# Performance work log

Hardware: AMD Instinct MI355X
Metric: run time of the kernel (lower is better)

## Reference

```python
import jax, jax.numpy as jnp
import numpy as np

N0, N1, N2, N3 = 262144, 65536, 16384, 4096
EPS = 1e-5  # BatchNorm1d default eps


def setup_inputs() -> dict:
    key = jax.random.key(0)
    ks = jax.random.split(key, 10)
    f0 = jax.random.normal(ks[0], (N0, 64), dtype=jnp.float32)
    f1 = jax.random.normal(ks[1], (N1, 128), dtype=jnp.float32)
    f2 = jax.random.normal(ks[2], (N2, 256), dtype=jnp.float32)
    f3 = jax.random.normal(ks[3], (N3, 512), dtype=jnp.float32)
    # upsampling indices: finer level gathers from coarser level
    idx0 = jax.random.randint(ks[4], (N2,), 0, N3, dtype=jnp.int32)   # f3 -> level2
    idx1 = jax.random.randint(ks[5], (N1,), 0, N2, dtype=jnp.int32)   # f2 -> level1
    idx2 = jax.random.randint(ks[6], (N0,), 0, N1, dtype=jnp.int32)   # f1 -> level0
    # BN weight init'd to constant 0.25 in the module; bias defaults to 0
    bn_w2, bn_b2 = jnp.full((512,), 0.25, jnp.float32), jnp.zeros((512,), jnp.float32)
    bn_w1, bn_b1 = jnp.full((256,), 0.25, jnp.float32), jnp.zeros((256,), jnp.float32)
    bn_w0, bn_b0 = jnp.full((128,), 0.25, jnp.float32), jnp.zeros((128,), jnp.float32)
    # Linear(in, out, bias=False) weights, torch layout [out, in]
    W2 = jax.random.normal(ks[7], (256, 512), dtype=jnp.float32) * 0.02
    W1 = jax.random.normal(ks[8], (128, 256), dtype=jnp.float32) * 0.02
    W0 = jax.random.normal(ks[9], (64, 128), dtype=jnp.float32) * 0.02
    return dict(f0=f0, f1=f1, f2=f2, f3=f3,
                bn_w2=bn_w2, bn_b2=bn_b2, W2=W2,
                bn_w1=bn_w1, bn_b1=bn_b1, W1=W1,
                bn_w0=bn_w0, bn_b0=bn_b0, W0=W0,
                idx0=idx0, idx1=idx1, idx2=idx2)


def _decode(f, bn_w, bn_b, W):
    # BatchNorm1d (training-mode batch stats, biased variance) -> Linear (no bias)
    mean = jnp.mean(f, axis=0)
    var = jnp.var(f, axis=0)
    xn = (f - mean) * jax.lax.rsqrt(var + EPS)
    return (xn * bn_w + bn_b) @ W.T  # [N, out_ch]


def reference(f0, f1, f2, f3, bn_w2, bn_b2, W2, bn_w1, bn_b1, W1,
              bn_w0, bn_b0, W0, idx0, idx1, idx2):
    # gather (upsample) -> BN -> Linear -> residual add, coarse to fine
    f2 = f2 + _decode(f3[idx0], bn_w2, bn_b2, W2)   # [N2, 256]
    f1 = f1 + _decode(f2[idx1], bn_w1, bn_b1, W1)   # [N1, 128]
    f0 = f0 + _decode(f1[idx2], bn_w0, bn_b0, W0)   # [N0, 64]
    return f0
```

## Files before the change

kernel.cpp:

```cpp
#include <hip/hip_runtime.h>
#include <hip/hip_cooperative_groups.h>

namespace cg = cooperative_groups;

#define BN_EPS 1e-5f

constexpr int PN0 = 262144, PN1 = 65536, PN2 = 16384, PN3 = 4096;
constexpr int NTHR = 256;
constexpr size_t MB = 1u << 20;

typedef __attribute__((ext_vector_type(8))) short short8;
typedef __attribute__((ext_vector_type(4))) float f32x4;
typedef __attribute__((ext_vector_type(4))) unsigned int u32x4;

typedef const __attribute__((address_space(1))) unsigned int gu32;
typedef __attribute__((address_space(3))) unsigned int lu32;

__device__ __forceinline__ unsigned f2bf(float f) {
    unsigned u = __builtin_bit_cast(unsigned, f);
    u += 0x7fff + ((u >> 16) & 1);
    return u >> 16;
}
__device__ __forceinline__ float bf2f(unsigned h) {
    return __builtin_bit_cast(float, h << 16);
}
__device__ __forceinline__ f32x4 ntload4(const float* p) {
    return __builtin_nontemporal_load(reinterpret_cast<const f32x4*>(p));
}
__device__ __forceinline__ void ntstore4(float* p, f32x4 v) {
    __builtin_nontemporal_store(v, reinterpret_cast<f32x4*>(p));
}

struct MegaArgs {
    const float *f0, *f1, *f2, *f3;
    const float *bnw2, *bnb2, *W2;
    const float *bnw1, *bnb1, *W1;
    const float *bnw0, *bnb0, *W0;
    const int *idx0, *idx1, *idx2;
    unsigned short *f3bf, *dec2, *dec1, *dec0, *f2p, *f1p, *Wp2, *Wp1, *Wp0;
    int *cnt2, *cnt1;
    float *part2, *part1, *part0;
    float *d2, *d1, *d0;
    float *out;
};

template<int G, int NL>
__device__ __forceinline__ void red_write(float* aux, const float s[8], const float q[8],
                                          int tid, int lr, int cgi,
                                          float* part, int vb, int C) {
    #pragma unroll
    for (int j = 0; j < 8; ++j) aux[(lr * G + cgi) * 8 + j] = s[j];
    __syncthreads();
    if (tid < G) {
        float ss[8] = {};
        for (int l = 0; l < NL; ++l)
            #pragma unroll
            for (int j = 0; j < 8; ++j) ss[j] += aux[(l * G + tid) * 8 + j];
        #pragma unroll
        for (int j = 0; j < 8; ++j)
            part[((size_t)vb * C + tid * 8 + j) * 2] = ss[j];
    }
    __syncthreads();
    #pragma unroll
    for (int j = 0; j < 8; ++j) aux[(lr * G + cgi) * 8 + j] = q[j];
    __syncthreads();
    if (tid < G) {
        float qq[8] = {};
        for (int l = 0; l < NL; ++l)
            #pragma unroll
            for (int j = 0; j < 8; ++j) qq[j] += aux[(l * G + tid) * 8 + j];
        #pragma unroll
        for (int j = 0; j < 8; ++j)
            part[((size_t)vb * C + tid * 8 + j) * 2 + 1] = qq[j];
    }
    __syncthreads();
}

__device__ void stats_gathered(const MegaArgs& a, int vb, int tid, float* aux) {
    const int cgi = tid & 63, lr = tid >> 6;
    const int r0 = vb * 128;
    float s[8] = {}, q[8] = {};
    for (int i = 0; i < 32; ++i) {
        int r = r0 + lr + 4 * i;
        int gi = a.idx0[r];
        const float* p = a.f3 + (size_t)gi * 512 + cgi * 8;
        float4 x0 = *reinterpret_cast<const float4*>(p);
        float4 x1 = *reinterpret_cast<const float4*>(p + 4);
        float v[8] = {x0.x, x0.y, x0.z, x0.w, x1.x, x1.y, x1.z, x1.w};
        #pragma unroll
        for (int j = 0; j < 8; ++j) { s[j] += v[j]; q[j] += v[j] * v[j]; }
    }
    red_write<64, 4>(aux, s, q, tid, lr, cgi, a.part2, vb, 512);
}

__device__ void cvt_f3(const MegaArgs& a, int vb, int tid) {
    const int cgi = tid & 63, lr = tid >> 6;
    const int r0 = vb * 32;
    #pragma unroll
    for (int i = 0; i < 8; ++i) {
        int r = r0 + lr + 4 * i;
        const float* p = a.f3 + (size_t)r * 512 + cgi * 8;
        float4 x0 = *reinterpret_cast<const float4*>(p);
        float4 x1 = *reinterpret_cast<const float4*>(p + 4);
        uint4 o;
        o.x = f2bf(x0.x) | (f2bf(x0.y) << 16);
        o.y = f2bf(x0.z) | (f2bf(x0.w) << 16);
        o.z = f2bf(x1.x) | (f2bf(x1.y) << 16);
        o.w = f2bf(x1.z) | (f2bf(x1.w) << 16);
        *reinterpret_cast<uint4*>(a.f3bf + (size_t)r * 512 + cgi * 8) = o;
    }
}

__device__ void phase1(const MegaArgs& a, int nb, int bid, int tid, float* aux) {
    for (int vb = bid; vb < 416; vb += nb) {
        if (vb < 128) {
            stats_gathered(a, vb, tid, aux);
        } else if (vb < 256) {
            cvt_f3(a, vb - 128, tid);
        } else if (vb < 288) {
            int b = vb - 256;
            #pragma unroll
            for (int i = 0; i < 8; ++i)
                atomicAdd(&a.cnt2[a.idx1[b * 2048 + i * NTHR + tid]], 1);
        } else {
            int b = vb - 288;
            #pragma unroll
            for (int i = 0; i < 8; ++i)
                atomicAdd(&a.cnt1[a.idx2[b * 2048 + i * NTHR + tid]], 1);
        }
    }
}

template<int K, int NB>
__device__ void prep_phase(int bid, int tid, const float* part,
                           const float* bnw, const float* bnb, float invN,
                           const float* W, unsigned short* Wp, float* d,
                           float* aux) {
    float* sc = aux;
    float* sh = aux + K;
    for (int c = tid; c < K; c += NTHR) {
        float s = 0.f, q = 0.f;
        for (int b = 0; b < NB; ++b) {
            float2 p = *reinterpret_cast<const float2*>(part + ((size_t)b * K + c) * 2);
            s += p.x;
            q += p.y;
        }
        float mean = s * invN;
        float var = fmaxf(q * invN - mean * mean, 0.f);
        float scl = bnw[c] * rsqrtf(var + BN_EPS);
        sc[c] = scl;
        sh[c] = bnb[c] - mean * scl;
    }
    __syncthreads();
    const int nl = tid >> 4;
    const int kc = tid & 15;
    const int n = bid * 16 + nl;
    const int cb = n >> 6, n64 = n & 63;
    const float* wrow = W + (size_t)n * K;
    unsigned short* wp = Wp + (size_t)cb * 64 * K;
    float dp = 0.f;
    #pragma unroll
    for (int i = 0; i < K / 128; ++i) {
        int k = kc * 8 + i * 128;
        float4 w0 = *reinterpret_cast<const float4*>(wrow + k);
        float4 w1 = *reinterpret_cast<const float4*>(wrow + k + 4);
        float4 s0 = *reinterpret_cast<const float4*>(&sc[k]);
        float4 s1 = *reinterpret_cast<const float4*>(&sc[k + 4]);
        float4 h0 = *reinterpret_cast<const float4*>(&sh[k]);
        float4 h1 = *reinterpret_cast<const float4*>(&sh[k + 4]);
        dp += h0.x * w0.x + h0.y * w0.y + h0.z * w0.z + h0.w * w0.w
            + h1.x * w1.x + h1.y * w1.y + h1.z * w1.z + h1.w * w1.w;
        uint4 o;
        o.x = f2bf(w0.x * s0.x) | (f2bf(w0.y * s0.y) << 16);
        o.y = f2bf(w0.z * s0.z) | (f2bf(w0.w * s0.w) << 16);
        o.z = f2bf(w1.x * s1.x) | (f2bf(w1.y * s1.y) << 16);
        o.w = f2bf(w1.z * s1.z) | (f2bf(w1.w * s1.w) << 16);
        int si = (n64 * K + k) ^ ((n64 & 7) << 3);
        *reinterpret_cast<uint4*>(wp + si) = o;
    }
    dp += __shfl_xor(dp, 1); dp += __shfl_xor(dp, 2);
    dp += __shfl_xor(dp, 4); dp += __shfl_xor(dp, 8);
    if (kc == 0) d[n] = dp;
    __syncthreads();
}

__device__ void gemm2_one(int chunk, int panel, int tid,
                          const unsigned short* src, const unsigned short* Wp,
                          const float* dvec, unsigned short* dec,
                          unsigned short* Wl) {
    constexpr int K = 512;
    const int lane = tid & 63;
    const int wv = tid >> 6;
    const int l15 = lane & 15, lg = lane >> 4;
    const char* gbase = (const char*)(Wp + (size_t)panel * 64 * K);
    char* lbase = (char*)Wl;

    #pragma unroll
    for (int i = 0; i < 8; ++i) {
        int ch = i * 4 + wv;
        __builtin_amdgcn_global_load_lds((gu32*)(gbase + ch * 1024 + lane * 16),
                                         (lu32*)(lbase + ch * 1024 + lane * 16), 16, 0, 0);
    }

    const int row = chunk * 64 + wv * 16 + l15;
    const unsigned short* xp = src + (size_t)row * K + lg * 8;
    short8 xf[16];
    #pragma unroll
    for (int kk = 0; kk < 16; ++kk)
        xf[kk] = *reinterpret_cast<const short8*>(xp + kk * 32);

    float4 dr[4];
    #pragma unroll
    for (int ni = 0; ni < 4; ++ni)
        dr[ni] = *reinterpret_cast<const float4*>(&dvec[panel * 64 + ni * 16 + lg * 4]);

    __syncthreads();

    f32x4 acc[4];
    #pragma unroll
    for (int ni = 0; ni < 4; ++ni) acc[ni] = (f32x4){0.f, 0.f, 0.f, 0.f};

    #pragma unroll
    for (int kk = 0; kk < 16; ++kk) {
        #pragma unroll
        for (int ni = 0; ni < 2; ++ni) {
            const int si = ((ni * 16 + l15) * K + kk * 32 + lg * 8) ^ ((l15 & 7) << 3);
            short8 wf = *reinterpret_cast<const short8*>(&Wl[si]);
            acc[ni] = __builtin_amdgcn_mfma_f32_16x16x32_bf16(wf, xf[kk], acc[ni], 0, 0, 0);
        }
    }
    __syncthreads();

    #pragma unroll
    for (int i = 0; i < 8; ++i) {
        int ch = i * 4 + wv;
        __builtin_amdgcn_global_load_lds((gu32*)(gbase + 32768 + ch * 1024 + lane * 16),
                                         (lu32*)(lbase + ch * 1024 + lane * 16), 16, 0, 0);
    }
    __syncthreads();

    #pragma unroll
    for (int kk = 0; kk < 16; ++kk) {
        #pragma unroll
        for (int ni = 0; ni < 2; ++ni) {
            const int si = ((ni * 16 + l15) * K + kk * 32 + lg * 8) ^ ((l15 & 7) << 3);
            short8 wf = *reinterpret_cast<const short8*>(&Wl[si]);
            acc[2 + ni] = __builtin_amdgcn_mfma_f32_16x16x32_bf16(wf, xf[kk], acc[2 + ni], 0, 0, 0);
        }
    }

    const size_t rowoff = (size_t)row * 256 + panel * 64;
    #pragma unroll
    for (int ni = 0; ni < 4; ++ni) {
        size_t off = rowoff + ni * 16 + lg * 4;
        float v0 = dr[ni].x + acc[ni][0];
        float v1 = dr[ni].y + acc[ni][1];
        float v2 = dr[ni].z + acc[ni][2];
        float v3 = dr[ni].w + acc[ni][3];
        *reinterpret_cast<uint2*>(&dec[off]) =
            make_uint2(f2bf(v0) | (f2bf(v1) << 16), f2bf(v2) | (f2bf(v3) << 16));
    }
    __syncthreads();
}

template<int K, int C>
__device__ void gemm_one(int chunk, int panel, int tid,
                         const unsigned short* src, const unsigned short* Wp,
                         const float* dvec, unsigned short* dec,
                         unsigned short* Wl) {
    constexpr int KK = K / 32;
    constexpr int CH = K / 8;
    const int lane = tid & 63;
    const int wv = tid >> 6;
    const int l15 = lane & 15, lg = lane >> 4;
    const int ncol0 = panel * 64;

    {
        const char* g = (const char*)(Wp + (size_t)panel * 64 * K);
        char* l = (char*)Wl;
        #pragma unroll
        for (int i = 0; i < CH / 4; ++i) {
            int ch = i * 4 + wv;
            __builtin_amdgcn_global_load_lds((gu32*)(g + ch * 1024 + lane * 16),
                                             (lu32*)(l + ch * 1024 + lane * 16), 16, 0, 0);
        }
    }

    const int row = chunk * 64 + wv * 16 + l15;
    const unsigned short* xp = src + (size_t)row * K + lg * 8;
    short8 xf[KK];
    #pragma unroll
    for (int kk = 0; kk < KK; ++kk)
        xf[kk] = *reinterpret_cast<const short8*>(xp + kk * 32);

    float4 dr[4];
    #pragma unroll
    for (int ni = 0; ni < 4; ++ni)
        dr[ni] = *reinterpret_cast<const float4*>(&dvec[ncol0 + ni * 16 + lg * 4]);

    __syncthreads();

    f32x4 acc[4];
    #pragma unroll
    for (int ni = 0; ni < 4; ++ni) acc[ni] = (f32x4){0.f, 0.f, 0.f, 0.f};
    #pragma unroll
    for (int kk = 0; kk < KK; ++kk) {
        #pragma unroll
        for (int ni = 0; ni < 4; ++ni) {
            const int si = ((ni * 16 + l15) * K + kk * 32 + lg * 8) ^ ((l15 & 7) << 3);
            short8 wf = *reinterpret_cast<const short8*>(&Wl[si]);
            acc[ni] = __builtin_amdgcn_mfma_f32_16x16x32_bf16(wf, xf[kk], acc[ni], 0, 0, 0);
        }
    }

    const size_t rowoff = (size_t)row * C + ncol0;
    #pragma unroll
    for (int ni = 0; ni < 4; ++ni) {
        size_t off = rowoff + ni * 16 + lg * 4;
        float v0 = dr[ni].x + acc[ni][0];
        float v1 = dr[ni].y + acc[ni][1];
        float v2 = dr[ni].z + acc[ni][2];
        float v3 = dr[ni].w + acc[ni][3];
        *reinterpret_cast<uint2*>(&dec[off]) =
            make_uint2(f2bf(v0) | (f2bf(v1) << 16), f2bf(v2) | (f2bf(v3) << 16));
    }
    __syncthreads();
}

__device__ void phase_gemm0(const MegaArgs& a, int nb, int bid, int tid, unsigned short* Wl) {
    constexpr int K = 128;
    const int lane = tid & 63;
    const int wv = tid >> 6;
    const int l15 = lane & 15, lg = lane >> 4;

    {
        const char* g = (const char*)a.Wp0;
        char* l = (char*)Wl;
        #pragma unroll
        for (int i = 0; i < 4; ++i) {
            int ch = i * 4 + wv;
            __builtin_amdgcn_global_load_lds((gu32*)(g + ch * 1024 + lane * 16),
                                             (lu32*)(l + ch * 1024 + lane * 16), 16, 0, 0);
        }
    }
    float4 dr[4];
    #pragma unroll
    for (int ni = 0; ni < 4; ++ni)
        dr[ni] = *reinterpret_cast<const float4*>(&a.d0[ni * 16 + lg * 4]);
    __syncthreads();

    for (int vb = bid; vb < 1024; vb += nb) {
        const int row = vb * 64 + wv * 16 + l15;
        const unsigned short* xp = a.f1p + (size_t)row * K + lg * 8;
        short8 xf[4];
        #pragma unroll
        for (int kk = 0; kk < 4; ++kk)
            xf[kk] = *reinterpret_cast<const short8*>(xp + kk * 32);
        f32x4 acc[4];
        #pragma unroll
        for (int ni = 0; ni < 4; ++ni) acc[ni] = (f32x4){0.f, 0.f, 0.f, 0.f};
        #pragma unroll
        for (int kk = 0; kk < 4; ++kk) {
            #pragma unroll
            for (int ni = 0; ni < 4; ++ni) {
                const int si = ((ni * 16 + l15) * K + kk * 32 + lg * 8) ^ ((l15 & 7) << 3);
                short8 wf = *reinterpret_cast<const short8*>(&Wl[si]);
                acc[ni] = __builtin_amdgcn_mfma_f32_16x16x32_bf16(wf, xf[kk], acc[ni], 0, 0, 0);
            }
        }
        const size_t rowoff = (size_t)row * 64;
        #pragma unroll
        for (int ni = 0; ni < 4; ++ni) {
            size_t off = rowoff + ni * 16 + lg * 4;
            float v0 = dr[ni].x + acc[ni][0];
            float v1 = dr[ni].y + acc[ni][1];
            float v2 = dr[ni].z + acc[ni][2];
            float v3 = dr[ni].w + acc[ni][3];
            *reinterpret_cast<uint2*>(&a.dec0[off]) =
                make_uint2(f2bf(v0) | (f2bf(v1) << 16), f2bf(v2) | (f2bf(v3) << 16));
        }
    }
}

template<int C, int IT, bool STATS, bool OUT_F32>
__device__ void ga_phase(int vb, int tid, const float* base,
                         const unsigned short* dec, const int* idx,
                         const int* cnt_next, void* outv, float* part,
                         float* aux) {
    constexpr int G = C / 8;
    constexpr int NL = 256 / G;
    const int cgi = tid % G;
    const int lr = tid / G;
    const int r0 = vb * (NL * IT);

    int g[IT];
    #pragma unroll
    for (int i = 0; i < IT; ++i) g[i] = idx[r0 + lr + NL * i];

    float wreg[IT];
    if constexpr (STATS) {
        #pragma unroll
        for (int i = 0; i < IT; ++i) wreg[i] = (float)cnt_next[r0 + lr + NL * i];
    }

    u32x4 dv[IT];
    #pragma unroll
    for (int i = 0; i < IT; ++i)
        dv[i] = *reinterpret_cast<const u32x4*>(dec + (size_t)g[i] * C + cgi * 8);

    f32x4 b0[IT], b1[IT];
    #pragma unroll
    for (int i = 0; i < IT; ++i) {
        const float* bp = base + (size_t)(r0 + lr + NL * i) * C + cgi * 8;
        b0[i] = ntload4(bp);
        b1[i] = ntload4(bp + 4);
    }

    float s[8] = {}, q[8] = {};
    #pragma unroll
    for (int i = 0; i < IT; ++i) {
        const int r = r0 + lr + NL * i;
        float v[8];
        v[0] = b0[i][0] + bf2f(dv[i][0] & 0xffffu);
        v[1] = b0[i][1] + bf2f(dv[i][0] >> 16);
        v[2] = b0[i][2] + bf2f(dv[i][1] & 0xffffu);
        v[3] = b0[i][3] + bf2f(dv[i][1] >> 16);
        v[4] = b1[i][0] + bf2f(dv[i][2] & 0xffffu);
        v[5] = b1[i][1] + bf2f(dv[i][2] >> 16);
        v[6] = b1[i][2] + bf2f(dv[i][3] & 0xffffu);
        v[7] = b1[i][3] + bf2f(dv[i][3] >> 16);
        if constexpr (OUT_F32) {
            float* op = (float*)outv + (size_t)r * C + cgi * 8;
            ntstore4(op, (f32x4){v[0], v[1], v[2], v[3]});
            ntstore4(op + 4, (f32x4){v[4], v[5], v[6], v[7]});
        } else {
            unsigned h[8];
            #pragma unroll
            for (int j = 0; j < 8; ++j) h[j] = f2bf(v[j]);
            u32x4 o = {h[0] | (h[1] << 16), h[2] | (h[3] << 16),
                       h[4] | (h[5] << 16), h[6] | (h[7] << 16)};
            *reinterpret_cast<u32x4*>((unsigned short*)outv + (size_t)r * C + cgi * 8) = o;
            if constexpr (STATS) {
                #pragma unroll
                for (int j = 0; j < 8; ++j) {
                    float rv = bf2f(h[j]);
                    s[j] += wreg[i] * rv;
                    q[j] += wreg[i] * rv * rv;
                }
            }
        }
    }

    if constexpr (STATS)
        red_write<G, NL>(aux, s, q, tid, lr, cgi, part, vb, C);
}

#define FENCE_SYNC { __threadfence(); gg.sync(); __threadfence(); }

__global__ __launch_bounds__(NTHR, 3) void mega(MegaArgs a) {
    __shared__ unsigned short Wl[64 * 256];
    __shared__ float aux[2048];
    cg::grid_group gg = cg::this_grid();
    const int nb = gridDim.x;
    const int bid = blockIdx.x;
    const int tid = threadIdx.x;

    phase1(a, nb, bid, tid, aux);
    FENCE_SYNC;

    for (int vb = bid; vb < 16; vb += nb)
        prep_phase<512, 128>(vb, tid, a.part2, a.bnw2, a.bnb2, 1.f / PN2, a.W2, a.Wp2, a.d2, aux);
    FENCE_SYNC;

    for (int vb = bid; vb < 256; vb += nb)
        gemm2_one(vb & 63, vb >> 6, tid, a.f3bf, a.Wp2, a.d2, a.dec2, Wl);
    FENCE_SYNC;

    for (int vb = bid; vb < 512; vb += nb)
        ga_phase<256, 4, true, false>(vb, tid, a.f2, a.dec2, a.idx0, a.cnt2, a.f2p, a.part1, aux);
    FENCE_SYNC;

    for (int vb = bid; vb < 8; vb += nb)
        prep_phase<256, 512>(vb, tid, a.part1, a.bnw1, a.bnb1, 1.f / PN1, a.W1, a.Wp1, a.d1, aux);
    FENCE_SYNC;

    for (int vb = bid; vb < 512; vb += nb)
        gemm_one<256, 128>(vb >> 1, vb & 1, tid, a.f2p, a.Wp1, a.d1, a.dec1, Wl);
    FENCE_SYNC;

    for (int vb = bid; vb < 512; vb += nb)
        ga_phase<128, 8, true, false>(vb, tid, a.f1, a.dec1, a.idx1, a.cnt1, a.f1p, a.part0, aux);
    FENCE_SYNC;

    for (int vb = bid; vb < 4; vb += nb)
        prep_phase<128, 512>(vb, tid, a.part0, a.bnw0, a.bnb0, 1.f / PN0, a.W0, a.Wp0, a.d0, aux);
    FENCE_SYNC;

    phase_gemm0(a, nb, bid, tid, Wl);
    FENCE_SYNC;

    for (int vb = bid; vb < 1024; vb += nb)
        ga_phase<64, 8, false, true>(vb, tid, a.f0, a.dec0, a.idx2, nullptr, a.out, nullptr, aux);
}

__global__ __launch_bounds__(NTHR) void k_p1(MegaArgs a) {
    __shared__ float aux[2048];
    phase1(a, gridDim.x, blockIdx.x, threadIdx.x, aux);
}
template<int K, int NB>
__global__ __launch_bounds__(NTHR) void k_prep(const float* part, const float* bnw,
                                               const float* bnb, float invN, const float* W,
                                               unsigned short* Wp, float* d) {
    __shared__ float aux[2048];
    prep_phase<K, NB>(blockIdx.x, threadIdx.x, part, bnw, bnb, invN, W, Wp, d, aux);
}
__global__ __launch_bounds__(NTHR) void k_gemm2(MegaArgs a) {
    __shared__ unsigned short Wl[64 * 256];
    for (int vb = blockIdx.x; vb < 256; vb += gridDim.x)
        gemm2_one(vb & 63, vb >> 6, threadIdx.x, a.f3bf, a.Wp2, a.d2, a.dec2, Wl);
}
__global__ __launch_bounds__(NTHR) void k_gemm1(MegaArgs a) {
    __shared__ unsigned short Wl[64 * 256];
    for (int vb = blockIdx.x; vb < 512; vb += gridDim.x)
        gemm_one<256, 128>(vb >> 1, vb & 1, threadIdx.x, a.f2p, a.Wp1, a.d1, a.dec1, Wl);
}
__global__ __launch_bounds__(NTHR) void k_gemm0(MegaArgs a) {
    __shared__ unsigned short Wl[64 * 128];
    phase_gemm0(a, gridDim.x, blockIdx.x, threadIdx.x, Wl);
}
__global__ __launch_bounds__(NTHR) void k_ga2(MegaArgs a) {
    __shared__ float aux[2048];
    for (int vb = blockIdx.x; vb < 512; vb += gridDim.x)
        ga_phase<256, 4, true, false>(vb, threadIdx.x, a.f2, a.dec2, a.idx0, a.cnt2,
                                      a.f2p, a.part1, aux);
}
__global__ __launch_bounds__(NTHR) void k_ga1(MegaArgs a) {
    __shared__ float aux[2048];
    for (int vb = blockIdx.x; vb < 512; vb += gridDim.x)
        ga_phase<128, 8, true, false>(vb, threadIdx.x, a.f1, a.dec1, a.idx1, a.cnt1,
                                      a.f1p, a.part0, aux);
}
__global__ __launch_bounds__(NTHR) void k_ga0(MegaArgs a) {
    for (int vb = blockIdx.x; vb < 1024; vb += gridDim.x)
        ga_phase<64, 8, false, true>(vb, threadIdx.x, a.f0, a.dec0, a.idx2, nullptr,
                                     a.out, nullptr, nullptr);
}

extern "C" void kernel_launch(void* const* d_in, const int* in_sizes, int n_in,
                              void* d_out, int out_size, void* d_ws, size_t ws_size,
                              hipStream_t stream) {
    char* wsb = (char*)d_ws;
    unsigned short* f3bf = (unsigned short*)wsb;
    unsigned short* dec2 = (unsigned short*)(wsb + 4 * MB);
    unsigned short* dec1 = (unsigned short*)(wsb + 6 * MB);
    unsigned short* dec0 = (unsigned short*)(wsb + 10 * MB);
    unsigned short* f2p  = (unsigned short*)(wsb + 18 * MB);
    unsigned short* f1p  = (unsigned short*)(wsb + 26 * MB);
    unsigned short* Wp2  = (unsigned short*)(wsb + 42 * MB);
    unsigned short* Wp1  = Wp2 + 4 * 64 * 512;
    unsigned short* Wp0  = Wp1 + 2 * 64 * 256;
    int* cnt2 = (int*)(Wp0 + 64 * 128);
    int* cnt1 = cnt2 + PN2;
    float* part2 = (float*)(cnt1 + PN1);
    float* part1 = part2 + 128 * 512 * 2;
    float* part0 = part1 + 512 * 256 * 2;
    float* d2 = part0 + 512 * 128 * 2;
    float* d1 = d2 + 256;
    float* d0 = d1 + 128;

    MegaArgs a;
    a.f0 = (const float*)d_in[0];
    a.f1 = (const float*)d_in[1];
    a.f2 = (const float*)d_in[2];
    a.f3 = (const float*)d_in[3];
    a.bnw2 = (const float*)d_in[4];
    a.bnb2 = (const float*)d_in[5];
    a.W2 = (const float*)d_in[6];
    a.bnw1 = (const float*)d_in[7];
    a.bnb1 = (const float*)d_in[8];
    a.W1 = (const float*)d_in[9];
    a.bnw0 = (const float*)d_in[10];
    a.bnb0 = (const float*)d_in[11];
    a.W0 = (const float*)d_in[12];
    a.idx0 = (const int*)d_in[13];
    a.idx1 = (const int*)d_in[14];
    a.idx2 = (const int*)d_in[15];
    a.f3bf = f3bf; a.dec2 = dec2; a.dec1 = dec1; a.dec0 = dec0;
    a.f2p = f2p; a.f1p = f1p; a.Wp2 = Wp2; a.Wp1 = Wp1; a.Wp0 = Wp0;
    a.cnt2 = cnt2; a.cnt1 = cnt1;
    a.part2 = part2; a.part1 = part1; a.part0 = part0;
    a.d2 = d2; a.d1 = d1; a.d0 = d0;
    a.out = (float*)d_out;

    hipMemsetAsync(cnt2, 0, (size_t)(PN2 + PN1) * sizeof(int), stream);

    int dev = 0;
    hipGetDevice(&dev);
    int coop = 0;
    hipDeviceGetAttribute(&coop, hipDeviceAttributeCooperativeLaunch, dev);
    int maxb = 0;
    hipOccupancyMaxActiveBlocksPerMultiprocessor(&maxb, mega, NTHR, 0);

    if (coop && maxb >= 1) {
        int nblk = maxb * 256;
        if (nblk > 1024) nblk = 1024;
        void* kargs[] = {&a};
        hipLaunchCooperativeKernel((void*)mega, dim3(nblk), dim3(NTHR), kargs, 0, stream);
    } else {
        k_p1<<<416, NTHR, 0, stream>>>(a);
        k_prep<512, 128><<<16, NTHR, 0, stream>>>(a.part2, a.bnw2, a.bnb2, 1.f / PN2, a.W2,
                                                  a.Wp2, a.d2);
        k_gemm2<<<256, NTHR, 0, stream>>>(a);
        k_ga2<<<512, NTHR, 0, stream>>>(a);
        k_prep<256, 512><<<8, NTHR, 0, stream>>>(a.part1, a.bnw1, a.bnb1, 1.f / PN1, a.W1,
                                                 a.Wp1, a.d1);
        k_gemm1<<<512, NTHR, 0, stream>>>(a);
        k_ga1<<<512, NTHR, 0, stream>>>(a);
        k_prep<128, 512><<<4, NTHR, 0, stream>>>(a.part0, a.bnw0, a.bnb0, 1.f / PN0, a.W0,
                                                 a.Wp0, a.d0);
        k_gemm0<<<768, NTHR, 0, stream>>>(a);
        k_ga0<<<1024, NTHR, 0, stream>>>(a);
    }
}
```

Baseline: 168.2 us.

## Fuse BN weight-prep into GEMM phases, drop three grid barriers

Removes the separate prep phases (and their grid-wide syncs) by having every GEMM block recompute BN scale/shift from partial sums and build its own bf16-scaled weight panel and bias vector directly in LDS. The GEMM2 panel width shrinks to 32 columns to give 512 work items, and the cooperative grid is fixed at 2 blocks per CU with launch bounds lowered from 3 to 2. This trades three grid barriers and a global Wp round-trip for redundant per-block stats reduction and weight conversion work.

Result: slower. 172.6 us (+2.6%).

```diff
diff --git a/kernel.cpp b/kernel.cpp
--- a/kernel.cpp
+++ b/kernel.cpp
@@ -12,9 +12,6 @@
 typedef __attribute__((ext_vector_type(8))) short short8;
 typedef __attribute__((ext_vector_type(4))) float f32x4;
 typedef __attribute__((ext_vector_type(4))) unsigned int u32x4;
-
-typedef const __attribute__((address_space(1))) unsigned int gu32;
-typedef __attribute__((address_space(3))) unsigned int lu32;
 
 __device__ __forceinline__ unsigned f2bf(float f) {
     unsigned u = __builtin_bit_cast(unsigned, f);
@@ -37,10 +34,9 @@
     const float *bnw1, *bnb1, *W1;
     const float *bnw0, *bnb0, *W0;
     const int *idx0, *idx1, *idx2;
-    unsigned short *f3bf, *dec2, *dec1, *dec0, *f2p, *f1p, *Wp2, *Wp1, *Wp0;
+    unsigned short *f3bf, *dec2, *dec1, *dec0, *f2p, *f1p;
     int *cnt2, *cnt1;
     float *part2, *part1, *part0;
-    float *d2, *d1, *d0;
     float *out;
 };
 
@@ -132,12 +128,8 @@
 }
 
 template<int K, int NB>
-__device__ void prep_phase(int bid, int tid, const float* part,
-                           const float* bnw, const float* bnb, float invN,
-                           const float* W, unsigned short* Wp, float* d,
-                           float* aux) {
-    float* sc = aux;
-    float* sh = aux + K;
+__device__ void calc_scsh(int tid, const float* part, const float* bnw, const float* bnb,
+                          float invN, float* sc, float* sh) {
     for (int c = tid; c < K; c += NTHR) {
         float s = 0.f, q = 0.f;
         for (int b = 0; b < NB; ++b) {
@@ -152,202 +144,196 @@
         sh[c] = bnb[c] - mean * scl;
     }
     __syncthreads();
-    const int nl = tid >> 4;
-    const int kc = tid & 15;
-    const int n = bid * 16 + nl;
-    const int cb = n >> 6, n64 = n & 63;
-    const float* wrow = W + (size_t)n * K;
-    unsigned short* wp = Wp + (size_t)cb * 64 * K;
-    float dp = 0.f;
-    #pragma unroll
-    for (int i = 0; i < K / 128; ++i) {
-        int k = kc * 8 + i * 128;
-        float4 w0 = *reinterpret_cast<const float4*>(wrow + k);
-        float4 w1 = *reinterpret_cast<const float4*>(wrow + k + 4);
-        float4 s0 = *reinterpret_cast<const float4*>(&sc[k]);
-        float4 s1 = *reinterpret_cast<const float4*>(&sc[k + 4]);
-        float4 h0 = *reinterpret_cast<const float4*>(&sh[k]);
-        float4 h1 = *reinterpret_cast<const float4*>(&sh[k + 4]);
-        dp += h0.x * w0.x + h0.y * w0.y + h0.z * w0.z + h0.w * w0.w
-            + h1.x * w1.x + h1.y * w1.y + h1.z * w1.z + h1.w * w1.w;
-        uint4 o;
-        o.x = f2bf(w0.x * s0.x) | (f2bf(w0.y * s0.y) << 16);
-        o.y = f2bf(w0.z * s0.z) | (f2bf(w0.w * s0.w) << 16);
-        o.z = f2bf(w1.x * s1.x) | (f2bf(w1.y * s1.y) << 16);
-        o.w = f2bf(w1.z * s1.z) | (f2bf(w1.w * s1.w) << 16);
-        int si = (n64 * K + k) ^ ((n64 & 7) << 3);
-        *reinterpret_cast<uint4*>(wp + si) = o;
-    }
-    dp += __shfl_xor(dp, 1); dp += __shfl_xor(dp, 2);
-    dp += __shfl_xor(dp, 4); dp += __shfl_xor(dp, 8);
-    if (kc == 0) d[n] = dp;
-    __syncthreads();
-}
-
-__device__ void gemm2_one(int chunk, int panel, int tid,
-                          const unsigned short* src, const unsigned short* Wp,
-                          const float* dvec, unsigned short* dec,
-                          unsigned short* Wl) {
+}
+
+__device__ void g2_phase(const MegaArgs& a, int nb, int bid, int tid,
+                         unsigned short* Wl, float* sc, float* sh, float* dl) {
     constexpr int K = 512;
+    calc_scsh<512, 128>(tid, a.part2, a.bnw2, a.bnb2, 1.f / PN2, sc, sh);
     const int lane = tid & 63;
     const int wv = tid >> 6;
     const int l15 = lane & 15, lg = lane >> 4;
-    const char* gbase = (const char*)(Wp + (size_t)panel * 64 * K);
-    char* lbase = (char*)Wl;
-
-    #pragma unroll
-    for (int i = 0; i < 8; ++i) {
-        int ch = i * 4 + wv;
-        __builtin_amdgcn_global_load_lds((gu32*)(gbase + ch * 1024 + lane * 16),
-                                         (lu32*)(lbase + ch * 1024 + lane * 16), 16, 0, 0);
-    }
-
-    const int row = chunk * 64 + wv * 16 + l15;
-    const unsigned short* xp = src + (size_t)row * K + lg * 8;
-    short8 xf[16];
-    #pragma unroll
-    for (int kk = 0; kk < 16; ++kk)
-        xf[kk] = *reinterpret_cast<const short8*>(xp + kk * 32);
-
-    float4 dr[4];
-    #pragma unroll
-    for (int ni = 0; ni < 4; ++ni)
-        dr[ni] = *reinterpret_cast<const float4*>(&dvec[panel * 64 + ni * 16 + lg * 4]);
-
-    __syncthreads();
-
-    f32x4 acc[4];
-    #pragma unroll
-    for (int ni = 0; ni < 4; ++ni) acc[ni] = (f32x4){0.f, 0.f, 0.f, 0.f};
-
-    #pragma unroll
-    for (int kk = 0; kk < 16; ++kk) {
+    const int n32 = tid >> 3, kc = tid & 7;
+
+    for (int vb = bid; vb < 512; vb += nb) {
+        const int chunk = vb & 63, panel = vb >> 6;
+        const int row = chunk * 64 + wv * 16 + l15;
+        const unsigned short* xp = a.f3bf + (size_t)row * K + lg * 8;
+        short8 xf[16];
+        #pragma unroll
+        for (int kk = 0; kk < 16; ++kk)
+            xf[kk] = *reinterpret_cast<const short8*>(xp + kk * 32);
+
+        {
+            const float* wrow = a.W2 + (size_t)(panel * 32 + n32) * K;
+            float dp = 0.f;
+            #pragma unroll
+            for (int i = 0; i < 8; ++i) {
+                int k = (kc + 8 * i) * 8;
+                float4 w0 = *reinterpret_cast<const float4*>(wrow + k);
+                float4 w1 = *reinterpret_cast<const float4*>(wrow + k + 4);
+                float4 s0 = *reinterpret_cast<const float4*>(&sc[k]);
+                float4 s1 = *reinterpret_cast<const float4*>(&sc[k + 4]);
+                float4 h0 = *reinterpret_cast<const float4*>(&sh[k]);
+                float4 h1 = *reinterpret_cast<const float4*>(&sh[k + 4]);
+                dp += h0.x * w0.x + h0.y * w0.y + h0.z * w0.z + h0.w * w0.w
+                    + h1.x * w1.x + h1.y * w1.y + h1.z * w1.z + h1.w * w1.w;
+                uint4 o;
+                o.x = f2bf(w0.x * s0.x) | (f2bf(w0.y * s0.y) << 16);
+                o.y = f2bf(w0.z * s0.z) | (f2bf(w0.w * s0.w) << 16);
+                o.z = f2bf(w1.x * s1.x) | (f2bf(w1.y * s1.y) << 16);
+                o.w = f2bf(w1.z * s1.z) | (f2bf(w1.w * s1.w) << 16);
+                int si = (n32 * K + k) ^ ((n32 & 7) << 3);
+                *reinterpret_cast<uint4*>(&Wl[si]) = o;
+            }
+            dp += __shfl_xor(dp, 1); dp += __shfl_xor(dp, 2); dp += __shfl_xor(dp, 4);
+            if (kc == 0) dl[n32] = dp;
+        }
+        __syncthreads();
+
+        f32x4 acc[2];
+        acc[0] = (f32x4){0.f, 0.f, 0.f, 0.f};
+        acc[1] = (f32x4){0.f, 0.f, 0.f, 0.f};
+        #pragma unroll
+        for (int kk = 0; kk < 16; ++kk) {
+            #pragma unroll
+            for (int ni = 0; ni < 2; ++ni) {
+                const int si = ((ni * 16 + l15) * K + kk * 32 + lg * 8) ^ ((l15 & 7) << 3);
+                short8 wf = *reinterpret_cast<const short8*>(&Wl[si]);
+                acc[ni] = __builtin_amdgcn_mfma_f32_16x16x32_bf16(wf, xf[kk], acc[ni], 0, 0, 0);
+            }
+        }
+
+        const size_t rowoff = (size_t)row * 256 + panel * 32;
         #pragma unroll
         for (int ni = 0; ni < 2; ++ni) {
-            const int si = ((ni * 16 + l15) * K + kk * 32 + lg * 8) ^ ((l15 & 7) << 3);
-            short8 wf = *reinterpret_cast<const short8*>(&Wl[si]);
-            acc[ni] = __builtin_amdgcn_mfma_f32_16x16x32_bf16(wf, xf[kk], acc[ni], 0, 0, 0);
-        }
-    }
-    __syncthreads();
-
-    #pragma unroll
-    for (int i = 0; i < 8; ++i) {
-        int ch = i * 4 + wv;
-        __builtin_amdgcn_global_load_lds((gu32*)(gbase + 32768 + ch * 1024 + lane * 16),
-                                         (lu32*)(lbase + ch * 1024 + lane * 16), 16, 0, 0);
-    }
-    __syncthreads();
-
-    #pragma unroll
-    for (int kk = 0; kk < 16; ++kk) {
-        #pragma unroll
-        for (int ni = 0; ni < 2; ++ni) {
-            const int si = ((ni * 16 + l15) * K + kk * 32 + lg * 8) ^ ((l15 & 7) << 3);
-            short8 wf = *reinterpret_cast<const short8*>(&Wl[si]);
-            acc[2 + ni] = __builtin_amdgcn_mfma_f32_16x16x32_bf16(wf, xf[kk], acc[2 + ni], 0, 0, 0);
-        }
-    }
-
-    const size_t rowoff = (size_t)row * 256 + panel * 64;
-    #pragma unroll
-    for (int ni = 0; ni < 4; ++ni) {
-        size_t off = rowoff + ni * 16 + lg * 4;
-        float v0 = dr[ni].x + acc[ni][0];
-        float v1 = dr[ni].y + acc[ni][1];
-        float v2 = dr[ni].z + acc[ni][2];
-        float v3 = dr[ni].w + acc[ni][3];
-        *reinterpret_cast<uint2*>(&dec[off]) =
-            make_uint2(f2bf(v0) | (f2bf(v1) << 16), f2bf(v2) | (f2bf(v3) << 16));
-    }
-    __syncthreads();
-}
-
-template<int K, int C>
-__device__ void gemm_one(int chunk, int panel, int tid,
-                         const unsigned short* src, const unsigned short* Wp,
-                         const float* dvec, unsigned short* dec,
-                         unsigned short* Wl) {
-    constexpr int KK = K / 32;
-    constexpr int CH = K / 8;
+            float4 dr = *reinterpret_cast<const float4*>(&dl[ni * 16 + lg * 4]);
+            size_t off = rowoff + ni * 16 + lg * 4;
+            float v0 = dr.x + acc[ni][0];
+            float v1 = dr.y + acc[ni][1];
+            float v2 = dr.z + acc[ni][2];
+            float v3 = dr.w + acc[ni][3];
+            *reinterpret_cast<uint2*>(&a.dec2[off]) =
+                make_uint2(f2bf(v0) | (f2bf(v1) << 16), f2bf(v2) | (f2bf(v3) << 16));
+        }
+        __syncthreads();
+    }
+}
+
+__device__ void g1_phase(const MegaArgs& a, int nb, int bid, int tid,
+                         unsigned short* Wl, float* sc, float* sh, float* dl) {
+    constexpr int K = 256;
+    calc_scsh<256, 512>(tid, a.part1, a.bnw1, a.bnb1, 1.f / PN1, sc, sh);
     const int lane = tid & 63;
     const int wv = tid >> 6;
     const int l15 = lane & 15, lg = lane >> 4;
-    const int ncol0 = panel * 64;
-
-    {
-        const char* g = (const char*)(Wp + (size_t)panel * 64 * K);
-        char* l = (char*)Wl;
-        #pragma unroll
-        for (int i = 0; i < CH / 4; ++i) {
-            int ch = i * 4 + wv;
-            __builtin_amdgcn_global_load_lds((gu32*)(g + ch * 1024 + lane * 16),
-                                             (lu32*)(l + ch * 1024 + lane * 16), 16, 0, 0);
-        }
-    }
-
-    const int row = chunk * 64 + wv * 16 + l15;
-    const unsigned short* xp = src + (size_t)row * K + lg * 8;
-    short8 xf[KK];
-    #pragma unroll
-    for (int kk = 0; kk < KK; ++kk)
-        xf[kk] = *reinterpret_cast<const short8*>(xp + kk * 32);
-
-    float4 dr[4];
-    #pragma unroll
-    for (int ni = 0; ni < 4; ++ni)
-        dr[ni] = *reinterpret_cast<const float4*>(&dvec[ncol0 + ni * 16 + lg * 4]);
-
-    __syncthreads();
-
-    f32x4 acc[4];
-    #pragma unroll
-    for (int ni = 0; ni < 4; ++ni) acc[ni] = (f32x4){0.f, 0.f, 0.f, 0.f};
-    #pragma unroll
-    for (int kk = 0; kk < KK; ++kk) {
+    const int n = tid >> 2, kc = tid & 3;
+
+    for (int vb = bid; vb < 512; vb += nb) {
+        const int chunk = vb & 255, panel = vb >> 8;
+        const int row = chunk * 64 + wv * 16 + l15;
+        const unsigned short* xp = a.f2p + (size_t)row * K + lg * 8;
+        short8 xf[8];
+        #pragma unroll
+        for (int kk = 0; kk < 8; ++kk)
+            xf[kk] = *reinterpret_cast<const short8*>(xp + kk * 32);
+
+        {
+            const float* wrow = a.W1 + (size_t)(panel * 64 + n) * K;
+            float dp = 0.f;
+            #pragma unroll
+            for (int i = 0; i < 8; ++i) {
+                int k = (kc + 4 * i) * 8;
+                float4 w0 = *reinterpret_cast<const float4*>(wrow + k);
+                float4 w1 = *reinterpret_cast<const float4*>(wrow + k + 4);
+                float4 s0 = *reinterpret_cast<const float4*>(&sc[k]);
+                float4 s1 = *reinterpret_cast<const float4*>(&sc[k + 4]);
+                float4 h0 = *reinterpret_cast<const float4*>(&sh[k]);
+                float4 h1 = *reinterpret_cast<const float4*>(&sh[k + 4]);
+                dp += h0.x * w0.x + h0.y * w0.y + h0.z * w0.z + h0.w * w0.w
+                    + h1.x * w1.x + h1.y * w1.y + h1.z * w1.z + h1.w * w1.w;
+                uint4 o;
+                o.x = f2bf(w0.x * s0.x) | (f2bf(w0.y * s0.y) << 16);
+                o.y = f2bf(w0.z * s0.z) | (f2bf(w0.w * s0.w) << 16);
+                o.z = f2bf(w1.x * s1.x) | (f2bf(w1.y * s1.y) << 16);
+                o.w = f2bf(w1.z * s1.z) | (f2bf(w1.w * s1.w) << 16);
+                int si = (n * K + k) ^ ((n & 7) << 3);
+                *reinterpret_cast<uint4*>(&Wl[si]) = o;
+            }
+            dp += __shfl_xor(dp, 1); dp += __shfl_xor(dp, 2);
+            if (kc == 0) dl[n] = dp;
+        }
+        __syncthreads();
+
+        f32x4 acc[4];
+        #pragma unroll
+        for (int ni = 0; ni < 4; ++ni) acc[ni] = (f32x4){0.f, 0.f, 0.f, 0.f};
+        #pragma unroll
+        for (int kk = 0; kk < 8; ++kk) {
+            #pragma unroll
+            for (int ni = 0; ni < 4; ++ni) {
+                const int si = ((ni * 16 + l15) * K + kk * 32 + lg * 8) ^ ((l15 & 7) << 3);
+                short8 wf = *reinterpret_cast<const short8*>(&Wl[si]);
+                acc[ni] = __builtin_amdgcn_mfma_f32_16x16x32_bf16(wf, xf[kk], acc[ni], 0, 0, 0);
+            }
+        }
+
+        const size_t rowoff = (size_t)row * 128 + panel * 64;
         #pragma unroll
         for (int ni = 0; ni < 4; ++ni) {
-            const int si = ((ni * 16 + l15) * K + kk * 32 + lg * 8) ^ ((l15 & 7) << 3);
-            short8 wf = *reinterpret_cast<const short8*>(&Wl[si]);
-            acc[ni] = __builtin_amdgcn_mfma_f32_16x16x32_bf16(wf, xf[kk], acc[ni], 0, 0, 0);
-        }
-    }
-
-    const size_t rowoff = (size_t)row * C + ncol0;
-    #pragma unroll
-    for (int ni = 0; ni < 4; ++ni) {
-        size_t off = rowoff + ni * 16 + lg * 4;
-        float v0 = dr[ni].x + acc[ni][0];
-        float v1 = dr[ni].y + acc[ni][1];
-        float v2 = dr[ni].z + acc[ni][2];
-        float v3 = dr[ni].w + acc[ni][3];
-        *reinterpret_cast<uint2*>(&dec[off]) =
-            make_uint2(f2bf(v0) | (f2bf(v1) << 16), f2bf(v2) | (f2bf(v3) << 16));
-    }
-    __syncthreads();
-}
-
-__device__ void phase_gemm0(const MegaArgs& a, int nb, int bid, int tid, unsigned short* Wl) {
+            float4 dr = *reinterpret_cast<const float4*>(&dl[ni * 16 + lg * 4]);
+            size_t off = rowoff + ni * 16 + lg * 4;
+            float v0 = dr.x + acc[ni][0];
+            float v1 = dr.y + acc[ni][1];
+            float v2 = dr.z + acc[ni][2];
+            float v3 = dr.w + acc[ni][3];
+            *reinterpret_cast<uint2*>(&a.dec1[off]) =
+                make_uint2(f2bf(v0) | (f2bf(v1) << 16), f2bf(v2) | (f2bf(v3) << 16));
+        }
+        __syncthreads();
+    }
+}
+
+__device__ void g0_phase(const MegaArgs& a, int nb, int bid, int tid,
+                         unsigned short* Wl, float* sc, float* sh, float* dl) {
     constexpr int K = 128;
+    calc_scsh<128, 512>(tid, a.part0, a.bnw0, a.bnb0, 1.f / PN0, sc, sh);
     const int lane = tid & 63;
     const int wv = tid >> 6;
     const int l15 = lane & 15, lg = lane >> 4;
+    const int n = tid >> 2, kc = tid & 3;
 
     {
-        const char* g = (const char*)a.Wp0;
-        char* l = (char*)Wl;
+        const float* wrow = a.W0 + (size_t)n * K;
+        float dp = 0.f;
         #pragma unroll
         for (int i = 0; i < 4; ++i) {
-            int ch = i * 4 + wv;
-            __builtin_amdgcn_global_load_lds((gu32*)(g + ch * 1024 + lane * 16),
-                                             (lu32*)(l + ch * 1024 + lane * 16), 16, 0, 0);
-        }
-    }
+            int k = (kc + 4 * i) * 8;
+            float4 w0 = *reinterpret_cast<const float4*>(wrow + k);
+            float4 w1 = *reinterpret_cast<const float4*>(wrow + k + 4);
+            float4 s0 = *reinterpret_cast<const float4*>(&sc[k]);
+            float4 s1 = *reinterpret_cast<const float4*>(&sc[k + 4]);
+            float4 h0 = *reinterpret_cast<const float4*>(&sh[k]);
+            float4 h1 = *reinterpret_cast<const float4*>(&sh[k + 4]);
+            dp += h0.x * w0.x + h0.y * w0.y + h0.z * w0.z + h0.w * w0.w
+                + h1.x * w1.x + h1.y * w1.y + h1.z * w1.z + h1.w * w1.w;
+            uint4 o;
+            o.x = f2bf(w0.x * s0.x) | (f2bf(w0.y * s0.y) << 16);
+            o.y = f2bf(w0.z * s0.z) | (f2bf(w0.w * s0.w) << 16);
+            o.z = f2bf(w1.x * s1.x) | (f2bf(w1.y * s1.y) << 16);
+            o.w = f2bf(w1.z * s1.z) | (f2bf(w1.w * s1.w) << 16);
+            int si = (n * K + k) ^ ((n & 7) << 3);
+            *reinterpret_cast<uint4*>(&Wl[si]) = o;
+        }
+        dp += __shfl_xor(dp, 1); dp += __shfl_xor(dp, 2);
+        if (kc == 0) dl[n] = dp;
+    }
+    __syncthreads();
+
     float4 dr[4];
     #pragma unroll
     for (int ni = 0; ni < 4; ++ni)
-        dr[ni] = *reinterpret_cast<const float4*>(&a.d0[ni * 16 + lg * 4]);
-    __syncthreads();
+        dr[ni] = *reinterpret_cast<const float4*>(&dl[ni * 16 + lg * 4]);
 
     for (int vb = bid; vb < 1024; vb += nb) {
         const int row = vb * 64 + wv * 16 + l15;
@@ -457,46 +443,34 @@
 
 #define FENCE_SYNC { __threadfence(); gg.sync(); __threadfence(); }
 
-__global__ __launch_bounds__(NTHR, 3) void mega(MegaArgs a) {
+__global__ __launch_bounds__(NTHR, 2) void mega(MegaArgs a) {
     __shared__ unsigned short Wl[64 * 256];
     __shared__ float aux[2048];
+    __shared__ float scsh[1088];
     cg::grid_group gg = cg::this_grid();
     const int nb = gridDim.x;
     const int bid = blockIdx.x;
     const int tid = threadIdx.x;
+    float* dl = scsh + 1024;
 
     phase1(a, nb, bid, tid, aux);
     FENCE_SYNC;
 
-    for (int vb = bid; vb < 16; vb += nb)
-        prep_phase<512, 128>(vb, tid, a.part2, a.bnw2, a.bnb2, 1.f / PN2, a.W2, a.Wp2, a.d2, aux);
-    FENCE_SYNC;
-
-    for (int vb = bid; vb < 256; vb += nb)
-        gemm2_one(vb & 63, vb >> 6, tid, a.f3bf, a.Wp2, a.d2, a.dec2, Wl);
+    g2_phase(a, nb, bid, tid, Wl, scsh, scsh + 512, dl);
     FENCE_SYNC;
 
     for (int vb = bid; vb < 512; vb += nb)
         ga_phase<256, 4, true, false>(vb, tid, a.f2, a.dec2, a.idx0, a.cnt2, a.f2p, a.part1, aux);
     FENCE_SYNC;
 
-    for (int vb = bid; vb < 8; vb += nb)
-        prep_phase<256, 512>(vb, tid, a.part1, a.bnw1, a.bnb1, 1.f / PN1, a.W1, a.Wp1, a.d1, aux);
-    FENCE_SYNC;
-
-    for (int vb = bid; vb < 512; vb += nb)
-        gemm_one<256, 128>(vb >> 1, vb & 1, tid, a.f2p, a.Wp1, a.d1, a.dec1, Wl);
+    g1_phase(a, nb, bid, tid, Wl, scsh, scsh + 256, dl);
     FENCE_SYNC;
 
     for (int vb = bid; vb < 512; vb += nb)
         ga_phase<128, 8, true, false>(vb, tid, a.f1, a.dec1, a.idx1, a.cnt1, a.f1p, a.part0, aux);
     FENCE_SYNC;
 
-    for (int vb = bid; vb < 4; vb += nb)
-        prep_phase<128, 512>(vb, tid, a.part0, a.bnw0, a.bnb0, 1.f / PN0, a.W0, a.Wp0, a.d0, aux);
-    FENCE_SYNC;
-
-    phase_gemm0(a, nb, bid, tid, Wl);
+    g0_phase(a, nb, bid, tid, Wl, scsh, scsh + 128, dl);
     FENCE_SYNC;
 
     for (int vb = bid; vb < 1024; vb += nb)
@@ -507,40 +481,34 @@
     __shared__ float aux[2048];
     phase1(a, gridDim.x, blockIdx.x, threadIdx.x, aux);
 }
-template<int K, int NB>
-__global__ __launch_bounds__(NTHR) void k_prep(const float* part, const float* bnw,
-                                               const float* bnb, float invN, const float* W,
-                                               unsigned short* Wp, float* d) {
-    __shared__ float aux[2048];
-    prep_phase<K, NB>(blockIdx.x, threadIdx.x, part, bnw, bnb, invN, W, Wp, d, aux);
-}
-__global__ __launch_bounds__(NTHR) void k_gemm2(MegaArgs a) {
+__global__ __launch_bounds__(NTHR) void k_g2(MegaArgs a) {
     __shared__ unsigned short Wl[64 * 256];
-    for (int vb = blockIdx.x; vb < 256; vb += gridDim.x)
-        gemm2_one(vb & 63, vb >> 6, threadIdx.x, a.f3bf, a.Wp2, a.d2, a.dec2, Wl);
-}
-__global__ __launch_bounds__(NTHR) void k_gemm1(MegaArgs a) {
+    __shared__ float scsh[1088];
+    g2_phase(a, gridDim.x, blockIdx.x, threadIdx.x, Wl, scsh, scsh + 512, scsh + 1024);
+}
+__global__ __launch_bounds__(NTHR) void k_g1(MegaArgs a) {
     __shared__ unsigned short Wl[64 * 256];
-    for (int vb = blockIdx.x; vb < 512; vb += gridDim.x)
-        gemm_one<256, 128>(vb >> 1, vb & 1, threadIdx.x, a.f2p, a.Wp1, a.d1, a.dec1, Wl);
-}
-__global__ __launch_bounds__(NTHR) void k_gemm0(MegaArgs a) {
+    __shared__ float scsh[1088];
+    g1_phase(a, gridDim.x, blockIdx.x, threadIdx.x, Wl, scsh, scsh + 256, scsh + 1024);
+}
+__global__ __launch_bounds__(NTHR) void k_g0(MegaArgs a) {
     __shared__ unsigned short Wl[64 * 128];
-    phase_gemm0(a, gridDim.x, blockIdx.x, threadIdx.x, Wl);
-}
-__global__ __launch_bounds__(NTHR) void k_ga2(MegaArgs a) {
+    __shared__ float scsh[1088];
+    g0_phase(a, gridDim.x, blockIdx.x, threadIdx.x, Wl, scsh, scsh + 128, scsh + 1024);
+}
+__global__ __launch_bounds__(NTHR) void k_a2(MegaArgs a) {
     __shared__ float aux[2048];
     for (int vb = blockIdx.x; vb < 512; vb += gridDim.x)
         ga_phase<256, 4, true, false>(vb, threadIdx.x, a.f2, a.dec2, a.idx0, a.cnt2,
                                       a.f2p, a.part1, aux);
 }
-__global__ __launch_bounds__(NTHR) void k_ga1(MegaArgs a) {
+__global__ __launch_bounds__(NTHR) void k_a1(MegaArgs a) {
     __shared__ float aux[2048];
     for (int vb = blockIdx.x; vb < 512; vb += gridDim.x)
         ga_phase<128, 8, true, false>(vb, threadIdx.x, a.f1, a.dec1, a.idx1, a.cnt1,
                                       a.f1p, a.part0, aux);
 }
-__global__ __launch_bounds__(NTHR) void k_ga0(MegaArgs a) {
+__global__ __launch_bounds__(NTHR) void k_a0(MegaArgs a) {
     for (int vb = blockIdx.x; vb < 1024; vb += gridDim.x)
         ga_phase<64, 8, false, true>(vb, threadIdx.x, a.f0, a.dec0, a.idx2, nullptr,
                                      a.out, nullptr, nullptr);
@@ -556,17 +524,11 @@
     unsigned short* dec0 = (unsigned short*)(wsb + 10 * MB);
     unsigned short* f2p  = (unsigned short*)(wsb + 18 * MB);
     unsigned short* f1p  = (unsigned short*)(wsb + 26 * MB);
-    unsigned short* Wp2  = (unsigned short*)(wsb + 42 * MB);
-    unsigned short* Wp1  = Wp2 + 4 * 64 * 512;
-    unsigned short* Wp0  = Wp1 + 2 * 64 * 256;
-    int* cnt2 = (int*)(Wp0 + 64 * 128);
+    int* cnt2 = (int*)(wsb + 42 * MB);
     int* cnt1 = cnt2 + PN2;
     float* part2 = (float*)(cnt1 + PN1);
     float* part1 = part2 + 128 * 512 * 2;
     float* part0 = part1 + 512 * 256 * 2;
-    float* d2 = part0 + 512 * 128 * 2;
-    float* d1 = d2 + 256;
-    float* d0 = d1 + 128;
 
     MegaArgs a;
     a.f0 = (const float*)d_in[0];
@@ -586,10 +548,9 @@
     a.idx1 = (const int*)d_in[14];
     a.idx2 = (const int*)d_in[15];
     a.f3bf = f3bf; a.dec2 = dec2; a.dec1 = dec1; a.dec0 = dec0;
-    a.f2p = f2p; a.f1p = f1p; a.Wp2 = Wp2; a.Wp1 = Wp1; a.Wp0 = Wp0;
+    a.f2p = f2p; a.f1p = f1p;
     a.cnt2 = cnt2; a.cnt1 = cnt1;
     a.part2 = part2; a.part1 = part1; a.part0 = part0;
-    a.d2 = d2; a.d1 = d1; a.d0 = d0;
     a.out = (float*)d_out;
 
     hipMemsetAsync(cnt2, 0, (size_t)(PN2 + PN1) * sizeof(int), stream);
@@ -602,23 +563,16 @@
     hipOccupancyMaxActiveBlocksPerMultiprocessor(&maxb, mega, NTHR, 0);
 
     if (coop && maxb >= 1) {
-        int nblk = maxb * 256;
-        if (nblk > 1024) nblk = 1024;
+        int nblk = (maxb >= 2 ? 2 : 1) * 256;
         void* kargs[] = {&a};
         hipLaunchCooperativeKernel((void*)mega, dim3(nblk), dim3(NTHR), kargs, 0, stream);
     } else {
         k_p1<<<416, NTHR, 0, stream>>>(a);
-        k_prep<512, 128><<<16, NTHR, 0, stream>>>(a.part2, a.bnw2, a.bnb2, 1.f / PN2, a.W2,
-                                                  a.Wp2, a.d2);
-        k_gemm2<<<256, NTHR, 0, stream>>>(a);
-        k_ga2<<<512, NTHR, 0, stream>>>(a);
-        k_prep<256, 512><<<8, NTHR, 0, stream>>>(a.part1, a.bnw1, a.bnb1, 1.f / PN1, a.W1,
-                                                 a.Wp1, a.d1);
-        k_gemm1<<<512, NTHR, 0, stream>>>(a);
-        k_ga1<<<512, NTHR, 0, stream>>>(a);
-        k_prep<128, 512><<<4, NTHR, 0, stream>>>(a.part0, a.bnw0, a.bnb0, 1.f / PN0, a.W0,
-                                                 a.Wp0, a.d0);
-        k_gemm0<<<768, NTHR, 0, stream>>>(a);
-        k_ga0<<<1024, NTHR, 0, stream>>>(a);
-    }
-}
+        k_g2<<<512, NTHR, 0, stream>>>(a);
+        k_a2<<<512, NTHR, 0, stream>>>(a);
+        k_g1<<<512, NTHR, 0, stream>>>(a);
+        k_a1<<<512, NTHR, 0, stream>>>(a);
+        k_g0<<<512, NTHR, 0, stream>>>(a);
+        k_a0<<<1024, NTHR, 0, stream>>>(a);
+    }
+}
```
